# Performance work log

Measured on AMD Instinct MI355X. Metric: run time of the kernel, lower is better.

Reference implementation:

```python
import jax, jax.numpy as jnp
import numpy as np

EPS = 1e-5
K = 20
LRELU = 0.2


def _bn(x, g, b, ch_axis):
    # inference BatchNorm with running_mean=0, running_var=1
    shape = [1] * x.ndim
    shape[ch_axis] = -1
    scale = (g / jnp.sqrt(1.0 + EPS)).reshape(shape)
    bias = b.reshape(shape)
    return x * scale + bias


def _lrelu(x):
    return jnp.where(x > 0, x, LRELU * x)


def _edge_conv(x, W, g, b):
    # x: (B, C, N) -> (B, C_out, N)
    B, C, N = x.shape
    xt = jnp.swapaxes(x, 1, 2)                      # (B, N, C)
    inner = -2.0 * jnp.einsum('bnc,bmc->bnm', xt, xt)
    xx = jnp.sum(xt * xt, axis=2)                   # (B, N)
    pdist = -xx[:, :, None] - inner - xx[:, None, :]  # negative sq dist (B,N,N)
    idx = jax.lax.top_k(pdist, K)[1]                # (B, N, K) nearest (incl. self)
    # gather neighbor features per batch: (C, N) indexed by (N, K) -> (C, N, K)
    neighbors = jax.vmap(lambda xf, id_: xf[:, id_])(x, idx)  # (B, C, N, K)
    center = jnp.broadcast_to(x[..., None], (B, C, N, K))
    edge = jnp.concatenate([center, neighbors - center], axis=1)  # (B, 2C, N, K)
    h = jnp.einsum('oc,bcnk->bonk', W, edge)        # 1x1 conv, no bias
    h = _lrelu(_bn(h, g, b, 1))
    return jnp.max(h, axis=-1)                      # (B, C_out, N)


def setup_inputs() -> dict:
    key = jax.random.key(0)
    ks = jax.random.split(key, 24)
    B, N = 4, 2048
    d = {}
    d['points'] = jax.random.normal(ks[0], (B, N, 3), dtype=jnp.float32)

    def w(k_, shape):
        return 0.1 * jax.random.normal(k_, shape, dtype=jnp.float32)

    def gam(k_, c):
        return 1.0 + 0.1 * jax.random.normal(k_, (c,), dtype=jnp.float32)

    def bet(k_, c):
        return 0.05 * jax.random.normal(k_, (c,), dtype=jnp.float32)

    # EdgeConv blocks: (out, 2*in)
    d['w1'], d['g1'], d['b1'] = w(ks[1], (64, 6)), gam(ks[2], 64), bet(ks[3], 64)
    d['w2'], d['g2'], d['b2'] = w(ks[4], (64, 128)), gam(ks[5], 64), bet(ks[6], 64)
    d['w3'], d['g3'], d['b3'] = w(ks[7], (128, 128)), gam(ks[8], 128), bet(ks[9], 128)
    d['w4'], d['g4'], d['b4'] = w(ks[10], (256, 256)), gam(ks[11], 256), bet(ks[12], 256)
    # conv5 1x1: 512 -> 1024
    d['w5'], d['g5'], d['b5'] = w(ks[13], (1024, 512)), gam(ks[14], 1024), bet(ks[15], 1024)
    # fc: 2048 -> 512 -> 256
    d['fw1'], d['fb1'] = w(ks[16], (512, 2048)), 0.05 * jax.random.normal(ks[17], (512,), dtype=jnp.float32)
    d['g6'], d['b6'] = gam(ks[18], 512), bet(ks[19], 512)
    d['fw2'], d['fb2'] = w(ks[20], (256, 512)), 0.05 * jax.random.normal(ks[21], (256,), dtype=jnp.float32)
    d['g7'], d['b7'] = gam(ks[22], 256), bet(ks[23], 256)
    return d


def reference(points, w1, g1, b1, w2, g2, b2, w3, g3, b3, w4, g4, b4,
              w5, g5, b5, fw1, fb1, g6, b6, fw2, fb2, g7, b7):
    x = jnp.swapaxes(points[:, :, :3], 1, 2)        # (B, 3, N)
    x1 = _edge_conv(x, w1, g1, b1)                  # (B, 64, N)
    x2 = _edge_conv(x1, w2, g2, b2)                 # (B, 64, N)
    x3 = _edge_conv(x2, w3, g3, b3)                 # (B, 128, N)
    x4 = _edge_conv(x3, w4, g4, b4)                 # (B, 256, N)
    h = jnp.concatenate([x1, x2, x3, x4], axis=1)   # (B, 512, N)
    h = _lrelu(_bn(jnp.einsum('oc,bcn->bon', w5, h), g5, b5, 1))  # (B, 1024, N)
    h_max = jnp.max(h, axis=-1)
    h_avg = jnp.mean(h, axis=-1)
    f = jnp.concatenate([h_max, h_avg], axis=1)     # (B, 2048)
    f = _lrelu(_bn(f @ fw1.T + fb1, g6, b6, 1))     # dropout = identity (eval)
    f = _bn(f @ fw2.T + fb2, g7, b7, 1)
    return f                                        # (B, 256)
```

## Files before the change

kernel.cpp:

```cpp
#include <hip/hip_runtime.h>
#include <hip/hip_bf16.h>
#include <float.h>

#define N_PTS 2048
#define B_SZ  4
#define KNN   20
#define LRELU_S 0.2f
#define FT    512
#define NPOOL 16

typedef __hip_bfloat16 bf16;
typedef __attribute__((ext_vector_type(8))) short short8v;
typedef __attribute__((ext_vector_type(4))) short short4v;
typedef __attribute__((ext_vector_type(4))) float floatx4;

__device__ __forceinline__ float b2f(const bf16 v) { return __bfloat162float(v); }
__device__ __forceinline__ float ldf(const float* p) { return *p; }
__device__ __forceinline__ float ldf(const bf16* p)  { return __bfloat162float(*p); }
__device__ __forceinline__ short8v ld8(const bf16* p) { return *(const short8v*)p; }
__device__ __forceinline__ unsigned umin(unsigned a, unsigned b) { return a < b ? a : b; }
__device__ __forceinline__ short bfbits(float f) {
    bf16 t = __float2bfloat16(f);
    return *reinterpret_cast<short*>(&t);
}
__device__ __forceinline__ unsigned short f2h(float f) {
    _Float16 h = (_Float16)f;
    return *reinterpret_cast<unsigned short*>(&h);
}
__device__ __forceinline__ float h2f(unsigned short u) {
    _Float16 h;
    *reinterpret_cast<unsigned short*>(&h) = u;
    return (float)h;
}

__device__ __forceinline__ void gload16(const void* g, void* l) {
    __builtin_amdgcn_global_load_lds(
        (const __attribute__((address_space(1))) void*)g,
        (__attribute__((address_space(3))) void*)l, 16, 0, 0);
}

__device__ __forceinline__ int sniff_body(const unsigned short* pts_hw) {
    int sane = 0;
    for (int j = 0; j < 64; ++j) {
        unsigned short v = pts_hw[2 * j];
        int e = (v >> 7) & 0xFF;
        if (e >= 100 && e <= 140) ++sane;
    }
    return (sane >= 32) ? 1 : 0;
}

__global__ void k_sniff(const unsigned short* __restrict__ pts_hw, int* __restrict__ flag) {
    if (threadIdx.x != 0 || blockIdx.x != 0) return;
    *flag = sniff_body(pts_hw);
}

struct WPack {
    const void* src[23];
    int off[24];
    int rows[23];
    int cols[23];
};

__device__ __forceinline__ void repack_body(const WPack& wp, int isb,
                                            float* __restrict__ dst, int i, int limit,
                                            int skip12) {
    if (i >= limit) return;
    int lo = 0, hi = 23;
    while (lo + 1 < hi) { int mid = (lo + hi) >> 1; if (i >= wp.off[mid]) lo = mid; else hi = mid; }
    if (skip12 && lo == 12) return;
    int j = i - wp.off[lo];
    float v = isb ? b2f(((const bf16*)wp.src[lo])[j]) : ((const float*)wp.src[lo])[j];
    int dj = j;
    int cols = wp.cols[lo];
    if (cols) dj = (j % cols) * wp.rows[lo] + (j / cols);
    dst[wp.off[lo] + dj] = v;
}

template<int C, int COUT>
__device__ __forceinline__ void wsplit_body(const void* __restrict__ W, int isb,
                                            bf16* __restrict__ dst, int i) {
    if (i >= COUT * C) return;
    int o = i / C, c = i % C;
    float w1 = isb ? b2f(((const bf16*)W)[(size_t)o * 2 * C + c])
                   : ((const float*)W)[(size_t)o * 2 * C + c];
    float w2 = isb ? b2f(((const bf16*)W)[(size_t)o * 2 * C + C + c])
                   : ((const float*)W)[(size_t)o * 2 * C + C + c];
    float wd = w1 - w2;
    bf16 h2 = __float2bfloat16(w2);
    bf16 hd = __float2bfloat16(wd);
    dst[i]                = h2;
    dst[COUT * C + i]     = __float2bfloat16(w2 - b2f(h2));
    dst[2 * COUT * C + i] = hd;
    dst[3 * COUT * C + i] = __float2bfloat16(wd - b2f(hd));
}

__device__ __forceinline__ void w5split_body(const void* __restrict__ W, int isb,
                                             bf16* __restrict__ dst, int i) {
    if (i >= 1024 * 512) return;
    float w = isb ? b2f(((const bf16*)W)[i]) : ((const float*)W)[i];
    bf16 h = __float2bfloat16(w);
    dst[i] = h;
    if (!isb) dst[1024 * 512 + i] = __float2bfloat16(w - b2f(h));
}

__device__ __forceinline__ void transpose_body(const void* __restrict__ pts, int isb,
                                               float* __restrict__ x0, int i) {
    if (i >= B_SZ * N_PTS) return;
    int b = i / N_PTS, n = i % N_PTS;
    for (int c = 0; c < 3; ++c) {
        size_t s = ((size_t)b * N_PTS + n) * 3 + c;
        float v = isb ? b2f(((const bf16*)pts)[s]) : ((const float*)pts)[s];
        x0[((size_t)b * 3 + c) * N_PTS + n] = v;
    }
}

__global__ void k_prep(WPack wp, float* __restrict__ wf, int rlimit,
                       const void* __restrict__ w2s, bf16* __restrict__ wsp2,
                       const void* __restrict__ w3s, bf16* __restrict__ wsp3,
                       const void* __restrict__ w4s, bf16* __restrict__ wsp4,
                       const void* __restrict__ w5s, bf16* __restrict__ w5sp,
                       const void* __restrict__ pts, float* __restrict__ x0,
                       int* __restrict__ flagout) {
    __shared__ int sfl;
    if (threadIdx.x == 0) {
        int f = sniff_body((const unsigned short*)pts);
        sfl = f;
        if (blockIdx.x == 0) *flagout = f;
    }
    __syncthreads();
    const int isb = sfl;
    const int nbrep = (rlimit + 255) >> 8;
    int ib = blockIdx.x, t = threadIdx.x;
    if (ib < nbrep) { repack_body(wp, isb, wf, ib * 256 + t, rlimit, 1); return; }
    ib -= nbrep;
    if (ib < 16)   { wsplit_body<64, 64>(w2s, isb, wsp2, ib * 256 + t); return; }
    ib -= 16;
    if (ib < 32)   { wsplit_body<64, 128>(w3s, isb, wsp3, ib * 256 + t); return; }
    ib -= 32;
    if (ib < 128)  { wsplit_body<128, 256>(w4s, isb, wsp4, ib * 256 + t); return; }
    ib -= 128;
    if (ib < 2048) { w5split_body(w5s, isb, w5sp, ib * 256 + t); return; }
    ib -= 2048;
    transpose_body(pts, isb, x0, ib * 256 + t);
}

__global__ void k_repack(WPack wp, const int* __restrict__ flag, float* __restrict__ dst, int limit) {
    repack_body(wp, *flag, dst, blockIdx.x * blockDim.x + threadIdx.x, limit, 0);
}
__global__ void k_transpose(const void* __restrict__ pts, const int* __restrict__ flag,
                            float* __restrict__ x0) {
    transpose_body(pts, *flag, x0, blockIdx.x * blockDim.x + threadIdx.x);
}

__device__ __forceinline__ void load32(const float* row, int mbase, float* r) {
    const float4* p = (const float4*)(row + mbase);
#pragma unroll
    for (int i = 0; i < 8; ++i) {
        float4 f = p[i];
        r[4 * i + 0] = f.x; r[4 * i + 1] = f.y; r[4 * i + 2] = f.z; r[4 * i + 3] = f.w;
    }
}
__device__ __forceinline__ void load32(const bf16* row, int mbase, float* r) {
    const uint4* p = (const uint4*)(row + mbase);
#pragma unroll
    for (int i = 0; i < 4; ++i) {
        uint4 u = p[i];
        r[8 * i + 0] = __uint_as_float(u.x << 16);
        r[8 * i + 1] = __uint_as_float(u.x & 0xFFFF0000u);
        r[8 * i + 2] = __uint_as_float(u.y << 16);
        r[8 * i + 3] = __uint_as_float(u.y & 0xFFFF0000u);
        r[8 * i + 4] = __uint_as_float(u.z << 16);
        r[8 * i + 5] = __uint_as_float(u.z & 0xFFFF0000u);
        r[8 * i + 6] = __uint_as_float(u.w << 16);
        r[8 * i + 7] = __uint_as_float(u.w & 0xFFFF0000u);
    }
}

__device__ __forceinline__ void s2ins(unsigned k, unsigned& m1, unsigned& m2) {
    unsigned lo = umin(m1, k);
    unsigned hi = (m1 < k) ? k : m1;
    m1 = lo;
    m2 = umin(m2, hi);
}

__device__ __forceinline__ void select20x2(const unsigned* ka, const unsigned* kb,
                                           int* outA, int* outB, int lane) {
    const unsigned SENT = 0xFFFFFFFFu;
    unsigned a1 = SENT, a2 = SENT, b1 = SENT, b2 = SENT;
#pragma unroll
    for (int j = 0; j < 32; ++j) {
        s2ins(ka[j], a1, a2);
        s2ins(kb[j], b1, b2);
    }
#pragma unroll 1
    for (int k = 0; k < KNN; ++k) {
        unsigned va = a1, vb = b1;
#pragma unroll
        for (int off = 32; off >= 1; off >>= 1) {
            va = umin(va, (unsigned)__shfl_xor((int)va, off));
            vb = umin(vb, (unsigned)__shfl_xor((int)vb, off));
        }
        if (lane == 0) { outA[k] = (int)(va & 2047u); outB[k] = (int)(vb & 2047u); }
        if (a1 == va) { a1 = a2; a2 = SENT; }
        if (b1 == vb) { b1 = b2; b2 = SENT; }
        if (a1 == SENT) {
#pragma unroll
            for (int j = 0; j < 32; ++j) {
                unsigned t = (ka[j] > va) ? ka[j] : SENT;
                s2ins(t, a1, a2);
            }
        }
        if (b1 == SENT) {
#pragma unroll
            for (int j = 0; j < 32; ++j) {
                unsigned t = (kb[j] > vb) ? kb[j] : SENT;
                s2ins(t, b1, b2);
            }
        }
    }
}

__global__ __launch_bounds__(256) void k_knn3ec(const float* __restrict__ x0,
        const float* __restrict__ Wt, const float* __restrict__ gam,
        const float* __restrict__ bet, bf16* __restrict__ featT,
        float* __restrict__ xxout) {
    __shared__ float qf[8][3];
    __shared__ int sidx[8][KNN];
    __shared__ float sh[8][KNN][3];
    int ib = blockIdx.x;
    int b  = ib / (N_PTS / 8);
    int q0 = (ib % (N_PTS / 8)) * 8;
    const float* xb = x0 + (size_t)b * 3 * N_PTS;

    if (threadIdx.x < 24) {
        int q = threadIdx.x / 3, c = threadIdx.x % 3;
        qf[q][c] = xb[(size_t)c * N_PTS + q0 + q];
    }
    __syncthreads();

    int w = threadIdx.x >> 6, lane = threadIdx.x & 63;
    int mbase = lane * 32;

    float da[32], db[32];
#pragma unroll
    for (int j = 0; j < 32; ++j) { da[j] = 0.f; db[j] = 0.f; }
#pragma unroll
    for (int c = 0; c < 3; ++c) {
        float r[32];
        load32(xb + (size_t)c * N_PTS, mbase, r);
        float qac = qf[2 * w][c], qbc = qf[2 * w + 1][c];
#pragma unroll
        for (int j = 0; j < 32; ++j) {
            float ta = r[j] - qac; da[j] = fmaf(ta, ta, da[j]);
            float tb = r[j] - qbc; db[j] = fmaf(tb, tb, db[j]);
        }
    }
    unsigned ka[32], kb[32];
#pragma unroll
    for (int j = 0; j < 32; ++j) {
        ka[j] = (__float_as_uint(da[j]) & 0xFFFFF800u) | (unsigned)(mbase + j);
        kb[j] = (__float_as_uint(db[j]) & 0xFFFFF800u) | (unsigned)(mbase + j);
    }
    select20x2(ka, kb, &sidx[2 * w][0], &sidx[2 * w + 1][0], lane);
    __syncthreads();

    for (int t = threadIdx.x; t < 8 * KNN * 3; t += 256) {
        int pt = t / (KNN * 3);
        int r  = t % (KNN * 3);
        int k = r / 3, c = r % 3;
        int m = sidx[pt][k] & (N_PTS - 1);
        sh[pt][k][c] = xb[(size_t)c * N_PTS + m];
    }
    __syncthreads();

    const float inv = rsqrtf(1.0f + 1e-5f);
    float scale = gam[lane] * inv, bias = bet[lane];
    float w1v[3], w2v[3];
#pragma unroll
    for (int c = 0; c < 3; ++c) {
        w1v[c] = Wt[(size_t)c * 64 + lane];
        w2v[c] = Wt[(size_t)(3 + c) * 64 + lane];
    }
#pragma unroll
    for (int p = 0; p < 2; ++p) {
        int pt = 2 * w + p;
        float base = 0.f;
#pragma unroll
        for (int c = 0; c < 3; ++c) base = fmaf(w1v[c] - w2v[c], qf[pt][c], base);
        float mx = -FLT_MAX;
#pragma unroll
        for (int k = 0; k < KNN; ++k) {
            float acc = 0.f;
#pragma unroll
            for (int c = 0; c < 3; ++c) acc = fmaf(w2v[c], sh[pt][k][c], acc);
            float h = (base + acc) * scale + bias;
            h = h > 0.f ? h : LRELU_S * h;
            mx = fmaxf(mx, h);
        }
        bf16 bv = __float2bfloat16(mx);
        size_t i = (size_t)b * N_PTS + q0 + pt;
        featT[i * FT + lane] = bv;
        float qv = b2f(bv);
        float s = qv * qv;
#pragma unroll
        for (int off = 32; off >= 1; off >>= 1) s += __shfl_xor(s, off);
        if (lane == 0) xxout[i] = s;
    }
}

template<typename T, int C>
__global__ __launch_bounds__(256) void k_knn(const T* __restrict__ x, int bstride,
                                             int* __restrict__ idx) {
    __shared__ float qf[4][C];
    int ib = blockIdx.x;
    int b  = ib / (N_PTS / 4);
    int q0 = (ib % (N_PTS / 4)) * 4;
    const T* xb = x + (size_t)b * bstride;

    for (int t = threadIdx.x; t < 4 * C; t += 256) {
        int pt = t / C, c = t % C;
        qf[pt][c] = ldf(&xb[(size_t)c * N_PTS + (q0 + pt)]);
    }
    __syncthreads();

    int w = threadIdx.x >> 6, lane = threadIdx.x & 63;
    int q = q0 + w;
    int mbase = lane * 32;

    float v[32];
#pragma unroll
    for (int j = 0; j < 32; ++j) v[j] = 0.f;

    for (int c = 0; c < C; ++c) {
        float qc = qf[w][c];
        float r[32];
        load32(xb + (size_t)c * N_PTS, mbase, r);
#pragma unroll
        for (int j = 0; j < 32; ++j) { float t = r[j] - qc; v[j] = fmaf(t, t, v[j]); }
    }

    for (int k = 0; k < KNN; ++k) {
        float bv = FLT_MAX; int bi = 0x7FFFFFFF;
#pragma unroll
        for (int j = 0; j < 32; ++j)
            if (v[j] < bv) { bv = v[j]; bi = mbase + j; }
#pragma unroll
        for (int off = 32; off >= 1; off >>= 1) {
            float ov = __shfl_xor(bv, off);
            int   oi = __shfl_xor(bi, off);
            if (ov < bv || (ov == bv && oi < bi)) { bv = ov; bi = oi; }
        }
        if (lane == 0) idx[((size_t)b * N_PTS + q) * KNN + k] = bi;
        int wl = bi >> 5, wj = bi & 31;
        if (lane == wl) {
#pragma unroll
            for (int j = 0; j < 32; ++j) if (j == wj) v[j] = FLT_MAX;
        }
    }
}

template<int C>
__device__ __forceinline__ void gram_body(const bf16* __restrict__ featT, int c0,
                                          const float* __restrict__ xx,
                                          unsigned short* __restrict__ D,
                                          short* lds, int ib) {
    const int KC = 64;
    short* At = lds;
    short* Bt = lds + 128 * 64;
    int b  = ib >> 8;
    int t  = ib & 255;
    int n0 = (t >> 4) << 7;
    int m0 = (t & 15) << 7;

    int tid = threadIdx.x;
    int w = tid >> 6, lane = tid & 63;
    int rw = (w & 1) * 64, cw = (w >> 1) * 64;
    int lrow = lane & 15, quad = lane >> 4;

    floatx4 acc[4][4];
#pragma unroll
    for (int ri = 0; ri < 4; ++ri)
#pragma unroll
        for (int ci = 0; ci < 4; ++ci) acc[ri][ci] = (floatx4){0.f, 0.f, 0.f, 0.f};

    for (int ck = 0; ck < C; ck += KC) {
        __syncthreads();
#pragma unroll
        for (int it = 0; it < 4; ++it) {
            int s = tid + it * 256;
            int row = s >> 3, seg = s & 7;
            int gseg = seg ^ (row & 7);
            gload16(featT + ((size_t)(b * N_PTS + n0 + row) * FT) + c0 + ck + gseg * 8,
                    &At[(s & ~63) * 8]);
            gload16(featT + ((size_t)(b * N_PTS + m0 + row) * FT) + c0 + ck + gseg * 8,
                    &Bt[(s & ~63) * 8]);
        }
        __syncthreads();
#pragma unroll
        for (int kk = 0; kk < KC; kk += 32) {
            int ks = kk >> 3;
            short8v a[4], bb[4];
#pragma unroll
            for (int ri = 0; ri < 4; ++ri) {
                int row = rw + ri * 16 + lrow;
                int seg = (ks + quad) ^ (row & 7);
                a[ri] = *(const short8v*)&At[row * 64 + seg * 8];
            }
#pragma unroll
            for (int ci = 0; ci < 4; ++ci) {
                int row = cw + ci * 16 + lrow;
                int seg = (ks + quad) ^ (row & 7);
                bb[ci] = *(const short8v*)&Bt[row * 64 + seg * 8];
            }
#pragma unroll
            for (int ri = 0; ri < 4; ++ri)
#pragma unroll
                for (int ci = 0; ci < 4; ++ci)
                    acc[ri][ci] = __builtin_amdgcn_mfma_f32_16x16x32_bf16(a[ri], bb[ci], acc[ri][ci], 0, 0, 0);
        }
    }

    const float* xr = xx + (size_t)b * N_PTS;
    float xmv[4];
#pragma unroll
    for (int ci = 0; ci < 4; ++ci)
        xmv[ci] = xr[m0 + cw + ci * 16 + lrow];
    float xnv[4][4];
#pragma unroll
    for (int ri = 0; ri < 4; ++ri)
#pragma unroll
        for (int reg = 0; reg < 4; ++reg)
            xnv[ri][reg] = xr[n0 + rw + ri * 16 + quad * 4 + reg];

    __syncthreads();
    unsigned short* dl = (unsigned short*)lds;
#pragma unroll
    for (int ri = 0; ri < 4; ++ri)
#pragma unroll
        for (int ci = 0; ci < 4; ++ci) {
            int ml = cw + ci * 16 + lrow;
#pragma unroll
            for (int reg = 0; reg < 4; ++reg) {
                int nl = rw + ri * 16 + quad * 4 + reg;
                float d = fmaf(-2.f, acc[ri][ci][reg], xmv[ci]) + xnv[ri][reg];
                d = fmaxf(d, 0.f);
                int col = (((ml >> 3) ^ (nl & 15)) << 3) + (ml & 7);
                dl[nl * 128 + col] = f2h(d);
            }
        }
    __syncthreads();
    unsigned short* Drow = D + ((size_t)b * N_PTS + n0) * N_PTS + m0;
#pragma unroll
    for (int it = 0; it < 8; ++it) {
        int ch = tid + it * 256;
        int row = ch >> 4;
        int c8 = (ch & 15) * 8;
        int g  = (((c8 >> 3) ^ (row & 15)) << 3);
        *(uint4*)(Drow + (size_t)row * N_PTS + c8) = *(const uint4*)(dl + row * 128 + g);
    }
}

template<int COUT, int C>
__device__ __forceinline__ void xform_body(const bf16* __restrict__ featT, int c0,
                                           const bf16* __restrict__ Wsp,
                                           bf16* __restrict__ Yh, int isb,
                                           short* lds, int ib2) {
    const int M2 = 2 * COUT;
    const int KC = 64;
    short* Bt = lds;
    int nt = ib2 & 63;
    int mt = ib2 >> 6;
    int tid = threadIdx.x;
    int w = tid >> 6, lane = tid & 63;
    int rw = (w & 1) * 64, cw = (w >> 1) * 64;
    int l15 = lane & 15, quad = lane >> 4;

    floatx4 acc[4][4];
#pragma unroll
    for (int ri = 0; ri < 4; ++ri)
#pragma unroll
        for (int ci = 0; ci < 4; ++ci) acc[ri][ci] = (floatx4){0.f, 0.f, 0.f, 0.f};

    for (int ck = 0; ck < C; ck += KC) {
        __syncthreads();
#pragma unroll
        for (int it = 0; it < 4; ++it) {
            int s = tid + it * 256;
            int row = s >> 3, seg = s & 7;
            int gseg = seg ^ (row & 7);
            gload16(featT + (size_t)(nt * 128 + row) * FT + c0 + ck + gseg * 8,
                    &Bt[(s & ~63) * 8]);
        }
        __syncthreads();
#pragma unroll
        for (int kk = 0; kk < KC; kk += 32) {
            int ks = kk >> 3;
            short8v bfr[4];
#pragma unroll
            for (int ci = 0; ci < 4; ++ci) {
                int row = cw + ci * 16 + l15;
                int seg = (ks + quad) ^ (row & 7);
                bfr[ci] = *(const short8v*)&Bt[row * 64 + seg * 8];
            }
#pragma unroll
            for (int ri = 0; ri < 4; ++ri) {
                int rbase = mt * 128 + rw + ri * 16;
                bool uselo = (!isb) || (rbase >= COUT);
                int mrow = rbase + l15;
                int base = (mrow < COUT) ? mrow : (mrow + COUT);
                const bf16* hi = Wsp + (size_t)base * C + ck + kk + quad * 8;
                short8v ah = ld8(hi);
                short8v al;
                if (uselo) al = ld8(hi + (size_t)COUT * C);
#pragma unroll
                for (int ci = 0; ci < 4; ++ci) {
                    acc[ri][ci] = __builtin_amdgcn_mfma_f32_16x16x32_bf16(ah, bfr[ci], acc[ri][ci], 0, 0, 0);
                    if (uselo)
                        acc[ri][ci] = __builtin_amdgcn_mfma_f32_16x16x32_bf16(al, bfr[ci], acc[ri][ci], 0, 0, 0);
                }
            }
        }
    }

    __syncthreads();
#pragma unroll
    for (int ri = 0; ri < 4; ++ri)
#pragma unroll
        for (int ci = 0; ci < 4; ++ci) {
            int nl = cw + ci * 16 + l15;
            int ml = rw + ri * 16 + quad * 4;
            short4v o4;
            o4[0] = bfbits(acc[ri][ci][0]);
            o4[1] = bfbits(acc[ri][ci][1]);
            o4[2] = bfbits(acc[ri][ci][2]);
            o4[3] = bfbits(acc[ri][ci][3]);
            int col = (((ml >> 3) ^ (nl & 15)) << 3) + (ml & 7);
            *(short4v*)&lds[nl * 128 + col] = o4;
        }
    __syncthreads();
    short* Ybase = (short*)Yh + (size_t)(nt * 128) * M2 + mt * 128;
#pragma unroll
    for (int it = 0; it < 8; ++it) {
        int ch = tid + it * 256;
        int row = ch >> 4;
        int c8 = (ch & 15) * 8;
        int g  = (((c8 >> 3) ^ (row & 15)) << 3);
        *(uint4*)(Ybase + (size_t)row * M2 + c8) = *(const uint4*)(lds + row * 128 + g);
    }
}

template<int C, int COUT>
__global__ __launch_bounds__(256) void k_gx(const bf16* __restrict__ featT, int c0,
        const bf16* __restrict__ Wsp, const float* __restrict__ xx,
        unsigned short* __restrict__ D, bf16* __restrict__ Yh,
        const int* __restrict__ flag) {
    __shared__ __align__(16) short lds[2 * 128 * 64];
    int ib = blockIdx.x;
    if (ib < B_SZ * 256) {
        gram_body<C>(featT, c0, xx, D, lds, ib);
    } else {
        xform_body<COUT, C>(featT, c0, Wsp, Yh, *flag, lds, ib - B_SZ * 256);
    }
}

template<int COUT>
__global__ __launch_bounds__(256) void k_selgmax(const unsigned short* __restrict__ D,
        const bf16* __restrict__ Yh,
        const float* __restrict__ gam, const float* __restrict__ bet,
        bf16* __restrict__ featT, int c0f, float* __restrict__ xxout) {
    const int M2 = 2 * COUT;
    const int OT = COUT / 64;
    __shared__ int sidx[8][KNN];

    int ib = blockIdx.x;
    int b  = ib / (N_PTS / 8);
    int q0 = (ib % (N_PTS / 8)) * 8;
    int w = threadIdx.x >> 6, lane = threadIdx.x & 63;
    int qa = q0 + 2 * w;
    const unsigned short* gA = D + ((size_t)b * N_PTS + qa) * N_PTS;
    const unsigned short* gB = gA + N_PTS;

    unsigned ka[32], kb[32];
#pragma unroll
    for (int r = 0; r < 4; ++r) {
        int m0 = r * 512 + (lane << 3);
        uint4 ua = *(const uint4*)(gA + m0);
        uint4 ub = *(const uint4*)(gB + m0);
        unsigned uw[4] = {ua.x, ua.y, ua.z, ua.w};
        unsigned vw[4] = {ub.x, ub.y, ub.z, ub.w};
#pragma unroll
        for (int h = 0; h < 4; ++h) {
            float a0 = h2f((unsigned short)(uw[h] & 0xFFFFu));
            float a1 = h2f((unsigned short)(uw[h] >> 16));
            ka[8 * r + 2 * h]     = (__float_as_uint(a0) & 0xFFFFF800u) | (unsigned)(m0 + 2 * h);
            ka[8 * r + 2 * h + 1] = (__float_as_uint(a1) & 0xFFFFF800u) | (unsigned)(m0 + 2 * h + 1);
            float c0v = h2f((unsigned short)(vw[h] & 0xFFFFu));
            float c1v = h2f((unsigned short)(vw[h] >> 16));
            kb[8 * r + 2 * h]     = (__float_as_uint(c0v) & 0xFFFFF800u) | (unsigned)(m0 + 2 * h);
            kb[8 * r + 2 * h + 1] = (__float_as_uint(c1v) & 0xFFFFF800u) | (unsigned)(m0 + 2 * h + 1);
        }
    }
    select20x2(ka, kb, &sidx[2 * w][0], &sidx[2 * w + 1][0], lane);
    __syncthreads();

    size_t iA = (size_t)b * N_PTS + qa;
    const float inv = rsqrtf(1.0f + 1e-5f);
    float yda[OT], ydb[OT], scl[OT], bis[OT], mxa[OT], mxb[OT];
#pragma unroll
    for (int j = 0; j < OT; ++j) {
        int o = lane + 64 * j;
        yda[j] = b2f(Yh[iA * M2 + COUT + o]);
        ydb[j] = b2f(Yh[(iA + 1) * M2 + COUT + o]);
        scl[j] = gam[o] * inv;
        bis[j] = bet[o];
        mxa[j] = -FLT_MAX; mxb[j] = -FLT_MAX;
    }
    const bf16* Yb = Yh + (size_t)b * N_PTS * M2;
#pragma unroll
    for (int k = 0; k < KNN; ++k) {
        int m0 = sidx[2 * w][k] & (N_PTS - 1);
        int m1 = sidx[2 * w + 1][k] & (N_PTS - 1);
        const bf16* r0 = Yb + (size_t)m0 * M2;
        const bf16* r1 = Yb + (size_t)m1 * M2;
#pragma unroll
        for (int j = 0; j < OT; ++j) {
            int o = lane + 64 * j;
            float ha = (yda[j] + b2f(r0[o])) * scl[j] + bis[j];
            ha = ha > 0.f ? ha : LRELU_S * ha;
            mxa[j] = fmaxf(mxa[j], ha);
            float hb = (ydb[j] + b2f(r1[o])) * scl[j] + bis[j];
            hb = hb > 0.f ? hb : LRELU_S * hb;
            mxb[j] = fmaxf(mxb[j], hb);
        }
    }
    float sa = 0.f, sb = 0.f;
#pragma unroll
    for (int j = 0; j < OT; ++j) {
        bf16 va = __float2bfloat16(mxa[j]);
        bf16 vb = __float2bfloat16(mxb[j]);
        featT[iA * FT + c0f + lane + 64 * j] = va;
        featT[(iA + 1) * FT + c0f + lane + 64 * j] = vb;
        if (xxout) {
            float pa = b2f(va); sa = fmaf(pa, pa, sa);
            float pb = b2f(vb); sb = fmaf(pb, pb, sb);
        }
    }
    if (xxout) {
#pragma unroll
        for (int off = 32; off >= 1; off >>= 1) {
            sa += __shfl_xor(sa, off);
            sb += __shfl_xor(sb, off);
        }
        if (lane == 0) { xxout[iA] = sa; xxout[iA + 1] = sb; }
    }
}

template<typename T, int C, int COUT, bool WF>
__global__ __launch_bounds__(256) void k_edgeconv(const T* __restrict__ x, int bstride,
                           const int* __restrict__ idx,
                           const float* __restrict__ Wt,
                           const float* __restrict__ gam,
                           const float* __restrict__ bet,
                           bf16* __restrict__ out, int ostride,
                           bf16* __restrict__ featT, int c0f,
                           float* __restrict__ xxout) {
    const int PT = 4;
    const int OT = COUT / 64;
    const int CP = (C + 3) & ~3;
    __shared__ float sh[PT][KNN + 1][CP];

    int ib = blockIdx.x;
    int b  = ib / (N_PTS / PT);
    int n0 = (ib % (N_PTS / PT)) * PT;
    const T* xb = x + (size_t)b * bstride;

    const int TOT = PT * (KNN + 1) * C;
    for (int t = threadIdx.x; t < TOT; t += 256) {
        int pt = t / ((KNN + 1) * C);
        int r  = t % ((KNN + 1) * C);
        int row = r / C, c = r % C;
        int n = n0 + pt;
        int m = (row == 0) ? n
                           : (idx[((size_t)b * N_PTS + n) * KNN + (row - 1)] & (N_PTS - 1));
        sh[pt][row][c] = ldf(&xb[(size_t)c * N_PTS + m]);
    }
    __syncthreads();

    int w = threadIdx.x >> 6, lane = threadIdx.x & 63;
    int n = n0 + w;

    constexpr int KT = (OT >= 4) ? 10 : 20;
    constexpr int NPASS = KNN / KT;

    float base[OT];
    float mx[OT];
#pragma unroll
    for (int j = 0; j < OT; ++j) { base[j] = 0.f; mx[j] = -FLT_MAX; }

    const float inv = rsqrtf(1.0f + 1e-5f);

#pragma unroll
    for (int pass = 0; pass < NPASS; ++pass) {
        float acc[OT][KT];
#pragma unroll
        for (int j = 0; j < OT; ++j)
#pragma unroll
            for (int k = 0; k < KT; ++k) acc[j][k] = 0.f;

        for (int c = 0; c < C; ++c) {
            float xq = sh[w][0][c];
            float w2v[OT];
#pragma unroll
            for (int j = 0; j < OT; ++j)
                w2v[j] = Wt[(size_t)(C + c) * COUT + lane + 64 * j];
            if (pass == 0) {
#pragma unroll
                for (int j = 0; j < OT; ++j) {
                    float w1v = Wt[(size_t)c * COUT + lane + 64 * j];
                    base[j] = fmaf(w1v - w2v[j], xq, base[j]);
                }
            }
#pragma unroll
            for (int k = 0; k < KT; ++k) {
                float nv = sh[w][1 + pass * KT + k][c];
#pragma unroll
                for (int j = 0; j < OT; ++j) acc[j][k] = fmaf(w2v[j], nv, acc[j][k]);
            }
        }

#pragma unroll
        for (int j = 0; j < OT; ++j) {
            int o = lane + 64 * j;
            float scale = gam[o] * inv, bias = bet[o];
#pragma unroll
            for (int k = 0; k < KT; ++k) {
                float h = (base[j] + acc[j][k]) * scale + bias;
                h = h > 0.f ? h : LRELU_S * h;
                mx[j] = fmaxf(mx[j], h);
            }
        }
    }

    float s = 0.f;
#pragma unroll
    for (int j = 0; j < OT; ++j) {
        int o = lane + 64 * j;
        bf16 bv = __float2bfloat16(mx[j]);
        if (!WF) out[(size_t)b * ostride + (size_t)o * N_PTS + n] = bv;
        if (WF) {
            featT[((size_t)b * N_PTS + n) * FT + c0f + o] = bv;
            float q = b2f(bv);
            s = fmaf(q, q, s);
        }
    }
    if (WF && xxout) {
#pragma unroll
        for (int off = 32; off >= 1; off >>= 1) s += __shfl_xor(s, off);
        if (lane == 0) xxout[(size_t)b * N_PTS + n] = s;
    }
}

__global__ __launch_bounds__(256) void k_conv5mfma(
        const bf16* __restrict__ featT, const bf16* __restrict__ w5sp,
        const float* __restrict__ g5, const float* __restrict__ b5,
        float* __restrict__ fmxp, float* __restrict__ fsmp,
        const int* __restrict__ flag) {
    __shared__ __align__(16) short Bt[128 * 64];
    __shared__ __align__(16) short Ah[64 * 64];
    __shared__ __align__(16) short Al[64 * 64];
    __shared__ float rmx[4][64];
    __shared__ float rsm[4][64];

    const int isb = *flag;
    int ib = blockIdx.x;
    int b  = ib / 256;
    int rem = ib % 256;
    int o0 = (rem >> 4) * 64;
    int nt = rem & 15;
    int tid = threadIdx.x;
    int w = tid >> 6, lane = tid & 63;
    int l15 = lane & 15, quad = lane >> 4;

    const bf16* Whi = w5sp;
    const bf16* Wlo = w5sp + 1024 * 512;
    const bf16* fb  = featT + (size_t)b * N_PTS * FT;
    const int nbase0 = nt * 128;

    floatx4 acc[4][2];
#pragma unroll
    for (int mi = 0; mi < 4; ++mi)
#pragma unroll
        for (int ni = 0; ni < 2; ++ni) acc[mi][ni] = (floatx4){0.f, 0.f, 0.f, 0.f};

    for (int ck = 0; ck < 512; ck += 64) {
        __syncthreads();
#pragma unroll
        for (int it = 0; it < 4; ++it) {
            int s = tid + it * 256;
            int row = s >> 3, seg = s & 7;
            int gseg = seg ^ (row & 7);
            gload16(fb + (size_t)(nbase0 + row) * FT + ck + gseg * 8,
                    &Bt[(s & ~63) * 8]);
        }
#pragma unroll
        for (int it = 0; it < 2; ++it) {
            int s = tid + it * 256;
            int row = s >> 3, seg = s & 7;
            int gseg = seg ^ (row & 7);
            gload16(Whi + (size_t)(o0 + row) * 512 + ck + gseg * 8, &Ah[(s & ~63) * 8]);
            if (!isb)
                gload16(Wlo + (size_t)(o0 + row) * 512 + ck + gseg * 8, &Al[(s & ~63) * 8]);
        }
        __syncthreads();
#pragma unroll
        for (int kk = 0; kk < 64; kk += 32) {
            int ks = kk >> 3;
            short8v bfr[2], ah[4], al[4];
#pragma unroll
            for (int ni = 0; ni < 2; ++ni) {
                int row = w * 32 + ni * 16 + l15;
                int seg = (ks + quad) ^ (row & 7);
                bfr[ni] = *(const short8v*)&Bt[row * 64 + seg * 8];
            }
#pragma unroll
            for (int mi = 0; mi < 4; ++mi) {
                int row = mi * 16 + l15;
                int seg = (ks + quad) ^ (row & 7);
                ah[mi] = *(const short8v*)&Ah[row * 64 + seg * 8];
                if (!isb) al[mi] = *(const short8v*)&Al[row * 64 + seg * 8];
            }
#pragma unroll
            for (int mi = 0; mi < 4; ++mi)
#pragma unroll
                for (int ni = 0; ni < 2; ++ni) {
                    acc[mi][ni] = __builtin_amdgcn_mfma_f32_16x16x32_bf16(ah[mi], bfr[ni], acc[mi][ni], 0, 0, 0);
                    if (!isb)
                        acc[mi][ni] = __builtin_amdgcn_mfma_f32_16x16x32_bf16(al[mi], bfr[ni], acc[mi][ni], 0, 0, 0);
                }
        }
    }

    const float inv = rsqrtf(1.0f + 1e-5f);
#pragma unroll
    for (int mi = 0; mi < 4; ++mi) {
#pragma unroll
        for (int r = 0; r < 4; ++r) {
            int o = o0 + mi * 16 + quad * 4 + r;
            float scale = g5[o] * inv, bias = b5[o];
            float mx = -FLT_MAX, sm = 0.f;
#pragma unroll
            for (int ni = 0; ni < 2; ++ni) {
                float h = acc[mi][ni][r] * scale + bias;
                h = h > 0.f ? h : LRELU_S * h;
                mx = fmaxf(mx, h);
                sm += h;
            }
#pragma unroll
            for (int off = 1; off <= 8; off <<= 1) {
                mx = fmaxf(mx, __shfl_xor(mx, off));
                sm += __shfl_xor(sm, off);
            }
            if (l15 == 0) {
                rmx[w][mi * 16 + quad * 4 + r] = mx;
                rsm[w][mi * 16 + quad * 4 + r] = sm;
            }
        }
    }
    __syncthreads();
    if (tid < 64) {
        float mx = -FLT_MAX, sm = 0.f;
#pragma unroll
        for (int ww = 0; ww < 4; ++ww) { mx = fmaxf(mx, rmx[ww][tid]); sm += rsm[ww][tid]; }
        fmxp[((size_t)b * 1024 + o0 + tid) * NPOOL + nt] = mx;
        fsmp[((size_t)b * 1024 + o0 + tid) * NPOOL + nt] = sm;
    }
}

__global__ void k_pool(const float* __restrict__ fmxp, const float* __restrict__ fsmp,
                       float* __restrict__ fvec) {
    int i = blockIdx.x * blockDim.x + threadIdx.x;
    if (i >= B_SZ * 1024) return;
    int b = i >> 10, o = i & 1023;
    float mx = -FLT_MAX, sm = 0.f;
    for (int ch = 0; ch < NPOOL; ++ch) {
        mx = fmaxf(mx, fmxp[(size_t)i * NPOOL + ch]);
        sm += fsmp[(size_t)i * NPOOL + ch];
    }
    fvec[(size_t)b * 2048 + o] = mx;
    fvec[(size_t)b * 2048 + 1024 + o] = sm * (1.0f / N_PTS);
}

__global__ __launch_bounds__(256) void k_fc1(const float* __restrict__ fvec,
        const void* __restrict__ fw1, const void* __restrict__ fb1,
        const void* __restrict__ g6,  const void* __restrict__ b6,
        const int* __restrict__ flag, float* __restrict__ tbuf) {
    __shared__ float red[4];
    int ib = blockIdx.x;
    int b = ib >> 9, o = ib & 511;
    const float* fv = fvec + (size_t)b * 2048;
    int tid = threadIdx.x;
    const int isb = *flag;
    float s = 0.f;
    if (isb) {
        const bf16* wr = (const bf16*)fw1 + (size_t)o * 2048;
        for (int j = tid; j < 2048; j += 256) s = fmaf(b2f(wr[j]), fv[j], s);
    } else {
        const float* wr = (const float*)fw1 + (size_t)o * 2048;
        for (int j = tid; j < 2048; j += 256) s = fmaf(wr[j], fv[j], s);
    }
#pragma unroll
    for (int off = 32; off >= 1; off >>= 1) s += __shfl_xor(s, off);
    if ((tid & 63) == 0) red[tid >> 6] = s;
    __syncthreads();
    if (tid == 0) {
        float fb = isb ? b2f(((const bf16*)fb1)[o]) : ((const float*)fb1)[o];
        float gg = isb ? b2f(((const bf16*)g6)[o])  : ((const float*)g6)[o];
        float bb = isb ? b2f(((const bf16*)b6)[o])  : ((const float*)b6)[o];
        float acc = fb + red[0] + red[1] + red[2] + red[3];
        float h = acc * gg * rsqrtf(1.0f + 1e-5f) + bb;
        tbuf[(size_t)b * 512 + o] = h > 0.f ? h : LRELU_S * h;
    }
}

__global__ __launch_bounds__(256) void k_fc2(const float* __restrict__ tbuf,
        const void* __restrict__ fw2, const void* __restrict__ fb2,
        const void* __restrict__ g7,  const void* __restrict__ b7,
        const int* __restrict__ flag, void* __restrict__ out) {
    __shared__ float red[4];
    int ib = blockIdx.x;
    int b = ib >> 8, o = ib & 255;
    const float* tv = tbuf + (size_t)b * 512;
    int tid = threadIdx.x;
    const int isb = *flag;
    float s;
    if (isb) {
        const bf16* wr = (const bf16*)fw2 + (size_t)o * 512;
        s = fmaf(b2f(wr[tid]), tv[tid], b2f(wr[tid + 256]) * tv[tid + 256]);
    } else {
        const float* wr = (const float*)fw2 + (size_t)o * 512;
        s = fmaf(wr[tid], tv[tid], wr[tid + 256] * tv[tid + 256]);
    }
#pragma unroll
    for (int off = 32; off >= 1; off >>= 1) s += __shfl_xor(s, off);
    if ((tid & 63) == 0) red[tid >> 6] = s;
    __syncthreads();
    if (tid == 0) {
        float fb = isb ? b2f(((const bf16*)fb2)[o]) : ((const float*)fb2)[o];
        float gg = isb ? b2f(((const bf16*)g7)[o])  : ((const float*)g7)[o];
        float bb = isb ? b2f(((const bf16*)b7)[o])  : ((const float*)b7)[o];
        float acc = fb + red[0] + red[1] + red[2] + red[3];
        float h = acc * gg * rsqrtf(1.0f + 1e-5f) + bb;
        if (isb) ((bf16*)out)[(size_t)b * 256 + o] = __float2bfloat16(h);
        else     ((float*)out)[(size_t)b * 256 + o] = h;
    }
}

#define NCH 2
__global__ __launch_bounds__(256) void k_conv5pool(const bf16* __restrict__ feat,
                            const float* __restrict__ w5,
                            const float* __restrict__ g5,
                            const float* __restrict__ b5,
                            float* __restrict__ fmxp, float* __restrict__ fsmp) {
    const int OT = 8;
    const int NT = 4;
    const int CHN = N_PTS / NCH;
    __shared__ float wl[OT][512];
    __shared__ float rmx[4][OT];
    __shared__ float rsm[4][OT];

    int ib = blockIdx.x;
    int ch = ib % NCH;
    int ot = (ib / NCH) % (1024 / OT);
    int b  = ib / (NCH * (1024 / OT));
    int o0 = ot * OT;
    const bf16* fb = feat + (size_t)b * 512 * N_PTS;

    for (int t = threadIdx.x; t < OT * 512; t += 256) {
        int o = t >> 9, c = t & 511;
        wl[o][c] = w5[(size_t)(o0 + o) * 512 + c];
    }
    __syncthreads();

    const int n0 = ch * CHN + threadIdx.x * NT;

    float acc[OT][NT];
#pragma unroll
    for (int o = 0; o < OT; ++o)
#pragma unroll
        for (int t = 0; t < NT; ++t) acc[o][t] = 0.f;

    for (int c = 0; c < 512; c += 4) {
        float fv[4][NT];
#pragma unroll
        for (int j = 0; j < 4; ++j) {
            uint2 u = *(const uint2*)(fb + (size_t)(c + j) * N_PTS + n0);
            fv[j][0] = __uint_as_float(u.x << 16);
            fv[j][1] = __uint_as_float(u.x & 0xFFFF0000u);
            fv[j][2] = __uint_as_float(u.y << 16);
            fv[j][3] = __uint_as_float(u.y & 0xFFFF0000u);
        }
#pragma unroll
        for (int o = 0; o < OT; ++o) {
            float4 wv = *(const float4*)&wl[o][c];
#pragma unroll
            for (int t = 0; t < NT; ++t) {
                acc[o][t] = fmaf(wv.x, fv[0][t], acc[o][t]);
                acc[o][t] = fmaf(wv.y, fv[1][t], acc[o][t]);
                acc[o][t] = fmaf(wv.z, fv[2][t], acc[o][t]);
                acc[o][t] = fmaf(wv.w, fv[3][t], acc[o][t]);
            }
        }
    }

    const float inv = rsqrtf(1.0f + 1e-5f);
    int w = threadIdx.x >> 6, lane = threadIdx.x & 63;
#pragma unroll
    for (int o = 0; o < OT; ++o) {
        float scale = g5[o0 + o] * inv, bias = b5[o0 + o];
        float mx = -FLT_MAX, sm = 0.f;
#pragma unroll
        for (int t = 0; t < NT; ++t) {
            float h = acc[o][t] * scale + bias;
            h = h > 0.f ? h : LRELU_S * h;
            mx = fmaxf(mx, h);
            sm += h;
        }
#pragma unroll
        for (int off = 32; off >= 1; off >>= 1) {
            mx = fmaxf(mx, __shfl_xor(mx, off));
            sm += __shfl_xor(sm, off);
        }
        if (lane == 0) { rmx[w][o] = mx; rsm[w][o] = sm; }
    }
    __syncthreads();
    if (threadIdx.x < OT) {
        int o = threadIdx.x;
        float mx = -FLT_MAX, sm = 0.f;
#pragma unroll
        for (int ww = 0; ww < 4; ++ww) { mx = fmaxf(mx, rmx[ww][o]); sm += rsm[ww][o]; }
        fmxp[((size_t)b * 1024 + o0 + o) * NCH + ch] = mx;
        fsmp[((size_t)b * 1024 + o0 + o) * NCH + ch] = sm;
    }
}

__global__ void k_head(const float* __restrict__ fmxp, const float* __restrict__ fsmp,
                       const float* __restrict__ fw1, const float* __restrict__ fb1,
                       const float* __restrict__ g6,  const float* __restrict__ b6,
                       const float* __restrict__ fw2, const float* __restrict__ fb2,
                       const float* __restrict__ g7,  const float* __restrict__ b7,
                       const int* __restrict__ flag, void* __restrict__ out) {
    __shared__ float f[2048];
    __shared__ float t[512];
    int b = blockIdx.x;
    for (int i = threadIdx.x; i < 1024; i += 256) {
        float mx = -FLT_MAX, sm = 0.f;
        for (int ch = 0; ch < NCH; ++ch) {
            mx = fmaxf(mx, fmxp[((size_t)b * 1024 + i) * NCH + ch]);
            sm += fsmp[((size_t)b * 1024 + i) * NCH + ch];
        }
        f[i]        = mx;
        f[1024 + i] = sm * (1.0f / N_PTS);
    }
    __syncthreads();
    const float inv = rsqrtf(1.0f + 1e-5f);
    for (int o = threadIdx.x; o < 512; o += 256) {
        const float* wr = fw1 + (size_t)o * 2048;
        float acc = fb1[o];
        for (int j = 0; j < 2048; ++j) acc += wr[j] * f[j];
        float h = acc * g6[o] * inv + b6[o];
        t[o] = h > 0.f ? h : LRELU_S * h;
    }
    __syncthreads();
    {
        int o = threadIdx.x;
        const float* wr = fw2 + (size_t)o * 512;
        float acc = fb2[o];
        for (int j = 0; j < 512; ++j) acc += wr[j] * t[j];
        float h = acc * g7[o] * inv + b7[o];
        if (*flag) ((bf16*)out)[(size_t)b * 256 + o] = __float2bfloat16(h);
        else       ((float*)out)[(size_t)b * 256 + o] = h;
    }
}

extern "C" void kernel_launch(void* const* d_in, const int* in_sizes, int n_in,
                              void* d_out, int out_size, void* d_ws, size_t ws_size,
                              hipStream_t stream) {
    static const int wsz[23] = {
        384, 64, 64,   8192, 64, 64,   16384, 128, 128,   65536, 256, 256,
        524288, 1024, 1024,   1048576, 512,   512, 512,   131072, 256,   256, 256
    };
    static const int trows[23] = {64,0,0, 64,0,0, 128,0,0, 256,0,0, 0,0,0, 0,0, 0,0, 0,0, 0,0};
    static const int tcols[23] = { 6,0,0,128,0,0, 128,0,0, 256,0,0, 0,0,0, 0,0, 0,0, 0,0, 0,0};

    WPack wp;
    int total = 0;
    for (int i = 0; i < 23; ++i) {
        wp.src[i] = d_in[i + 1]; wp.off[i] = total; total += wsz[i];
        wp.rows[i] = trows[i]; wp.cols[i] = tcols[i];
    }
    wp.off[23] = total;

    const size_t flag_bytes = 16;
    const size_t x0_bytes   = (size_t)B_SZ * 3 * N_PTS * 4;
    const size_t feat_bytes = (size_t)B_SZ * 512 * N_PTS * 2;
    const size_t idx_bytes  = (size_t)B_SZ * N_PTS * KNN * 4;
    const size_t pool_bytes = (size_t)B_SZ * 1024 * 4 * 2;
    const size_t wf_bytes   = (size_t)total * 4;
    const size_t base_need  = flag_bytes + x0_bytes + feat_bytes + idx_bytes + pool_bytes + wf_bytes;

    const size_t featT_bytes = (size_t)B_SZ * N_PTS * FT * 2;
    const size_t xx_bytes    = (size_t)B_SZ * N_PTS * 4;
    const size_t wsp2_elems  = 4 * 64 * 64;
    const size_t wsp3_elems  = 4 * 128 * 64;
    const size_t wsp4_elems  = 4 * 256 * 128;
    const size_t w5sp_elems  = 2 * 1024 * 512;
    const size_t wsp_bytes   = (wsp2_elems + wsp3_elems + wsp4_elems + w5sp_elems) * 2;
    const size_t Yh_bytes    = (size_t)B_SZ * N_PTS * 512 * 2;
    const size_t S_bytes     = (size_t)B_SZ * N_PTS * N_PTS * 2;
    const size_t full_need   = base_need + featT_bytes + 2 * xx_bytes + wsp_bytes
                             + Yh_bytes + S_bytes;

    if (ws_size < base_need) return;
    const bool use_gram = (ws_size >= full_need);

    char* w = (char*)d_ws;
    int*   flag = (int*)w;              w += flag_bytes;
    float* x0   = (float*)w;            w += x0_bytes;
    bf16*  feat = (bf16*)w;             w += feat_bytes;
    int*   idx  = (int*)w;              w += idx_bytes;
    w += pool_bytes;
    float* wf   = (float*)w;            w += wf_bytes;
    bf16*  featT = (bf16*)w;            w += featT_bytes;
    float* xxA   = (float*)w;           w += xx_bytes;
    float* xxB   = (float*)w;           w += xx_bytes;
    bf16*  wsp2  = (bf16*)w;            w += wsp2_elems * 2;
    bf16*  wsp3  = (bf16*)w;            w += wsp3_elems * 2;
    bf16*  wsp4  = (bf16*)w;            w += wsp4_elems * 2;
    bf16*  w5sp  = (bf16*)w;            w += w5sp_elems * 2;
    bf16*  Yh    = (bf16*)w;            w += Yh_bytes;
    unsigned short* D = (unsigned short*)w;

    float* fmxp = (float*)idx;
    float* fsmp = fmxp + (size_t)B_SZ * 1024 * NPOOL;
    float* fvec = fsmp + (size_t)B_SZ * 1024 * NPOOL;
    float* tbuf = fvec + (size_t)B_SZ * 2048;

    const int FBS = 512 * N_PTS;

    const float* w1t = wf + wp.off[0],  *g1 = wf + wp.off[1],  *b1 = wf + wp.off[2];
    const float* w2t = wf + wp.off[3],  *g2 = wf + wp.off[4],  *b2 = wf + wp.off[5];
    const float* w3t = wf + wp.off[6],  *g3 = wf + wp.off[7],  *b3 = wf + wp.off[8];
    const float* w4t = wf + wp.off[9],  *g4 = wf + wp.off[10], *b4 = wf + wp.off[11];
    const float* w5  = wf + wp.off[12], *g5 = wf + wp.off[13], *b5 = wf + wp.off[14];
    const float* fw1 = wf + wp.off[15], *fb1 = wf + wp.off[16];
    const float* g6  = wf + wp.off[17], *b6 = wf + wp.off[18];
    const float* fw2 = wf + wp.off[19], *fb2 = wf + wp.off[20];
    const float* g7  = wf + wp.off[21], *b7 = wf + wp.off[22];

    const int GK = B_SZ * N_PTS / 4;
    const int G8 = B_SZ * N_PTS / 8;
    const int NG = B_SZ * 256;

    if (use_gram) {
        const int rlimit = wp.off[15];
        const int nbrep = (rlimit + 255) / 256;
        const int prep_grid = nbrep + 16 + 32 + 128 + 2048 + 32;
        k_prep<<<prep_grid, 256, 0, stream>>>(wp, wf, rlimit,
                                              d_in[4], wsp2, d_in[7], wsp3,
                                              d_in[10], wsp4, d_in[13], w5sp,
                                              d_in[0], x0, flag);

        k_knn3ec<<<G8, 256, 0, stream>>>(x0, w1t, g1, b1, featT, xxA);
        k_gx<64, 64><<<NG + 64, 256, 0, stream>>>(featT, 0, wsp2, xxA, D, Yh, flag);
        k_selgmax<64><<<G8, 256, 0, stream>>>(D, Yh, g2, b2, featT, 64, xxB);
        k_gx<64, 128><<<NG + 128, 256, 0, stream>>>(featT, 64, wsp3, xxB, D, Yh, flag);
        k_selgmax<128><<<G8, 256, 0, stream>>>(D, Yh, g3, b3, featT, 128, xxA);
        k_gx<128, 256><<<NG + 256, 256, 0, stream>>>(featT, 128, wsp4, xxA, D, Yh, flag);
        k_selgmax<256><<<G8, 256, 0, stream>>>(D, Yh, g4, b4, featT, 256, nullptr);

        k_conv5mfma<<<B_SZ * 256, 256, 0, stream>>>(featT, w5sp, g5, b5, fmxp, fsmp, flag);
        k_pool<<<(B_SZ * 1024 + 255) / 256, 256, 0, stream>>>(fmxp, fsmp, fvec);
        k_fc1<<<B_SZ * 512, 256, 0, stream>>>(fvec, d_in[16], d_in[17], d_in[18], d_in[19],
                                              flag, tbuf);
        k_fc2<<<B_SZ * 256, 256, 0, stream>>>(tbuf, d_in[20], d_in[21], d_in[22], d_in[23],
                                              flag, d_out);
    } else {
        k_sniff<<<1, 64, 0, stream>>>((const unsigned short*)d_in[0], flag);
        k_repack<<<(total + 255) / 256, 256, 0, stream>>>(wp, flag, wf, total);
        k_transpose<<<(B_SZ * N_PTS + 255) / 256, 256, 0, stream>>>(d_in[0], flag, x0);

        k_knn<float, 3><<<GK, 256, 0, stream>>>(x0, 3 * N_PTS, idx);
        k_edgeconv<float, 3, 64, false><<<GK, 256, 0, stream>>>(
            x0, 3 * N_PTS, idx, w1t, g1, b1, feat + 0 * N_PTS, FBS, nullptr, 0, nullptr);
        k_knn<bf16, 64><<<GK, 256, 0, stream>>>(feat + 0 * N_PTS, FBS, idx);
        k_edgeconv<bf16, 64, 64, false><<<GK, 256, 0, stream>>>(
            feat + 0 * N_PTS, FBS, idx, w2t, g2, b2, feat + 64 * N_PTS, FBS, nullptr, 0, nullptr);
        k_knn<bf16, 64><<<GK, 256, 0, stream>>>(feat + 64 * N_PTS, FBS, idx);
        k_edgeconv<bf16, 64, 128, false><<<GK, 256, 0, stream>>>(
            feat + 64 * N_PTS, FBS, idx, w3t, g3, b3, feat + 128 * N_PTS, FBS, nullptr, 0, nullptr);
        k_knn<bf16, 128><<<GK, 256, 0, stream>>>(feat + 128 * N_PTS, FBS, idx);
        k_edgeconv<bf16, 128, 256, false><<<GK, 256, 0, stream>>>(
            feat + 128 * N_PTS, FBS, idx, w4t, g4, b4, feat + 256 * N_PTS, FBS, nullptr, 0, nullptr);

        k_conv5pool<<<B_SZ * (1024 / 8) * NCH, 256, 0, stream>>>(feat, w5, g5, b5, fmxp, fsmp);
        k_head<<<B_SZ, 256, 0, stream>>>(fmxp, fsmp, fw1, fb1, g6, b6, fw2, fb2, g7, b7,
                                         flag, d_out);
    }
}
```

Baseline: 326.5 us.

## Exploit Gram distance symmetry by computing only upper-triangular tiles

```diff
diff --git a/kernel.cpp b/kernel.cpp
--- a/kernel.cpp
+++ b/kernel.cpp
@@ -8,6 +8,7 @@
 #define LRELU_S 0.2f
 #define FT    512
 #define NPOOL 16
+#define NTRI  136
 
 typedef __hip_bfloat16 bf16;
 typedef __attribute__((ext_vector_type(8))) short short8v;
@@ -367,10 +368,13 @@
     const int KC = 64;
     short* At = lds;
     short* Bt = lds + 128 * 64;
-    int b  = ib >> 8;
-    int t  = ib & 255;
-    int n0 = (t >> 4) << 7;
-    int m0 = (t & 15) << 7;
+    int b = ib / NTRI;
+    int t = ib % NTRI;
+    int ti = 0;
+    while (t >= 16 - ti) { t -= 16 - ti; ++ti; }
+    int tj = ti + t;
+    int n0 = ti << 7;
+    int m0 = tj << 7;
 
     int tid = threadIdx.x;
     int w = tid >> 6, lane = tid & 63;
@@ -442,21 +446,53 @@
 #pragma unroll
             for (int reg = 0; reg < 4; ++reg) {
                 int nl = rw + ri * 16 + quad * 4 + reg;
-                float d = fmaf(-2.f, acc[ri][ci][reg], xmv[ci]) + xnv[ri][reg];
+                float d = fmaf(-2.f, acc[ri][ci][reg], xmv[ci] + xnv[ri][reg]);
                 d = fmaxf(d, 0.f);
                 int col = (((ml >> 3) ^ (nl & 15)) << 3) + (ml & 7);
                 dl[nl * 128 + col] = f2h(d);
             }
         }
     __syncthreads();
-    unsigned short* Drow = D + ((size_t)b * N_PTS + n0) * N_PTS + m0;
-#pragma unroll
-    for (int it = 0; it < 8; ++it) {
-        int ch = tid + it * 256;
-        int row = ch >> 4;
-        int c8 = (ch & 15) * 8;
-        int g  = (((c8 >> 3) ^ (row & 15)) << 3);
-        *(uint4*)(Drow + (size_t)row * N_PTS + c8) = *(const uint4*)(dl + row * 128 + g);
+    {
+        unsigned short* Drow = D + ((size_t)b * N_PTS + n0) * N_PTS + m0;
+#pragma unroll
+        for (int it = 0; it < 8; ++it) {
+            int ch = tid + it * 256;
+            int row = ch >> 4;
+            int c8 = (ch & 15) * 8;
+            int g  = (((c8 >> 3) ^ (row & 15)) << 3);
+            *(uint4*)(Drow + (size_t)row * N_PTS + c8) = *(const uint4*)(dl + row * 128 + g);
+        }
+    }
+
+    if (ti == tj) return;
+
+    __syncthreads();
+#pragma unroll
+    for (int ri = 0; ri < 4; ++ri)
+#pragma unroll
+        for (int ci = 0; ci < 4; ++ci) {
+            int ml = cw + ci * 16 + lrow;
+#pragma unroll
+            for (int reg = 0; reg < 4; ++reg) {
+                int nl = rw + ri * 16 + quad * 4 + reg;
+                float d = fmaf(-2.f, acc[ri][ci][reg], xmv[ci] + xnv[ri][reg]);
+                d = fmaxf(d, 0.f);
+                int col = (((nl >> 3) ^ (ml & 15)) << 3) + (nl & 7);
+                dl[ml * 128 + col] = f2h(d);
+            }
+        }
+    __syncthreads();
+    {
+        unsigned short* Drow = D + ((size_t)b * N_PTS + m0) * N_PTS + n0;
+#pragma unroll
+        for (int it = 0; it < 8; ++it) {
+            int ch = tid + it * 256;
+            int row = ch >> 4;
+            int c8 = (ch & 15) * 8;
+            int g  = (((c8 >> 3) ^ (row & 15)) << 3);
+            *(uint4*)(Drow + (size_t)row * N_PTS + c8) = *(const uint4*)(dl + row * 128 + g);
+        }
     }
 }
 
@@ -556,10 +592,10 @@
         const int* __restrict__ flag) {
     __shared__ __align__(16) short lds[2 * 128 * 64];
     int ib = blockIdx.x;
-    if (ib < B_SZ * 256) {
+    if (ib < B_SZ * NTRI) {
         gram_body<C>(featT, c0, xx, D, lds, ib);
     } else {
-        xform_body<COUT, C>(featT, c0, Wsp, Yh, *flag, lds, ib - B_SZ * 256);
+        xform_body<COUT, C>(featT, c0, Wsp, Yh, *flag, lds, ib - B_SZ * NTRI);
     }
 }
 
@@ -1159,7 +1195,7 @@
 
     const int GK = B_SZ * N_PTS / 4;
     const int G8 = B_SZ * N_PTS / 8;
-    const int NG = B_SZ * 256;
+    const int NG = B_SZ * NTRI;
 
     if (use_gram) {
         const int rlimit = wp.off[15];
```

Result: no change. 323.5 us (-0.9%).
